# Kernel optimization log

Hardware: AMD Instinct MI355X
Metric: run time of the kernel (lower is better)

## Reference

```python
import jax, jax.numpy as jnp
import numpy as np

LN_EPS = 1e-5


def _layernorm(x, gamma, beta):
    mu = jnp.mean(x, axis=-1, keepdims=True)
    var = jnp.mean(jnp.square(x - mu), axis=-1, keepdims=True)
    return (x - mu) * jax.lax.rsqrt(var + LN_EPS) * gamma + beta


def setup_inputs() -> dict:
    key = jax.random.key(0)
    ks = jax.random.split(key, 8)
    B, T, C, H, HS = 8, 2048, 384, 6, 64
    s = C ** -0.5
    return {
        "x": jax.random.normal(ks[0], (B, T, C), jnp.float32),
        "wq": jax.random.normal(ks[1], (H, C, HS), jnp.float32) * s,
        "wk": jax.random.normal(ks[2], (H, C, HS), jnp.float32) * s,
        "wv": jax.random.normal(ks[3], (H, C, HS), jnp.float32) * s,
        "w_proj": jax.random.normal(ks[4], (C, C), jnp.float32) * s,
        "b_proj": jnp.zeros((C,), jnp.float32),
        "w1": jax.random.normal(ks[5], (C, 4 * C), jnp.float32) * s,
        "b1": jnp.zeros((4 * C,), jnp.float32),
        "w2": jax.random.normal(ks[6], (4 * C, C), jnp.float32) * (4 * C) ** -0.5,
        "b2": jnp.zeros((C,), jnp.float32),
        "g1": jnp.ones((C,), jnp.float32),
        "be1": jnp.zeros((C,), jnp.float32),
        "g2": jnp.ones((C,), jnp.float32),
        "be2": jnp.zeros((C,), jnp.float32),
    }


def reference(x, wq, wk, wv, w_proj, b_proj, w1, b1, w2, b2, g1, be1, g2, be2):
    B, T, C = x.shape
    HS = wq.shape[-1]
    # --- multi-head causal self-attention (per-head linear, concat, proj) ---
    q = jnp.einsum("btc,hcd->bhtd", x, wq)
    k = jnp.einsum("btc,hcd->bhtd", x, wk)
    v = jnp.einsum("btc,hcd->bhtd", x, wv)
    scores = jnp.einsum("bhtd,bhsd->bhts", q, k) * (HS ** -0.5)
    causal = jnp.tril(jnp.ones((T, T), bool))
    scores = jnp.where(causal, scores, -jnp.inf)
    att = jax.nn.softmax(scores, axis=-1)  # dropout = identity (eval)
    o = jnp.einsum("bhts,bhsd->bhtd", att, v)
    o = o.transpose(0, 2, 1, 3).reshape(B, T, C)  # concat heads
    sa = o @ w_proj + b_proj
    # --- post-LN residual ---
    x = _layernorm(x + sa, g1, be1)
    # --- feed-forward ---
    ff = jax.nn.relu(x @ w1 + b1) @ w2 + b2
    x = _layernorm(x + ff, g2, be2)
    return x
```

## Files before the change

### kernel.cpp

```cpp
#include <hip/hip_runtime.h>

typedef unsigned short u16;
typedef unsigned int u32;
typedef u16 u16x4 __attribute__((ext_vector_type(4)));
typedef u16 u16x8 __attribute__((ext_vector_type(8)));
typedef u32 u32x4 __attribute__((ext_vector_type(4)));
typedef __bf16 bf16v8 __attribute__((ext_vector_type(8)));
typedef float f32x4 __attribute__((ext_vector_type(4)));
typedef float f32x2 __attribute__((ext_vector_type(2)));

#define DEV __device__ __forceinline__

DEV u16 f2bf(float f) {
  union { float f; u32 u; } v; v.f = f;
  u32 r = v.u + 0x7fffu + ((v.u >> 16) & 1u);
  return (u16)(r >> 16);
}
DEV float bf2f(u16 u) { union { u32 u; float f; } v; v.u = ((u32)u) << 16; return v.f; }

DEV u32 cvtpk(float a, float b) {
  u32 d;
  asm("v_cvt_pk_bf16_f32 %0, %1, %2" : "=v"(d) : "v"(a), "v"(b));
  return d;
}

DEV f32x4 mfma16(u16x8 a, u16x8 b, f32x4 c) {
  return __builtin_amdgcn_mfma_f32_16x16x32_bf16(
      __builtin_bit_cast(bf16v8, a), __builtin_bit_cast(bf16v8, b), c, 0, 0, 0);
}

typedef const __attribute__((address_space(1))) void* gas_ptr;
typedef __attribute__((address_space(3))) void* las_ptr;
#define GLOAD16(GP, LP) __builtin_amdgcn_global_load_lds((gas_ptr)(GP), (las_ptr)(LP), 16, 0, 0)

__global__ __launch_bounds__(256) void cast_x_kernel(const float* __restrict__ x,
                                                     u16* __restrict__ xb) {
  int i = blockIdx.x * 256 + threadIdx.x;
  const f32x4* p = (const f32x4*)x;
  f32x4 a = p[2 * i], b = p[2 * i + 1];
  u16x8 o;
  #pragma unroll
  for (int j = 0; j < 4; ++j) { o[j] = f2bf(a[j]); o[4 + j] = f2bf(b[j]); }
  *((u16x8*)xb + i) = o;
}

__global__ __launch_bounds__(256) void prep_w_kernel(
    const float* __restrict__ wq, const float* __restrict__ wk,
    const float* __restrict__ wv, const float* __restrict__ wproj,
    const float* __restrict__ w1, const float* __restrict__ w2,
    u16* __restrict__ wqkvt, u16* __restrict__ wprojt,
    u16* __restrict__ w1t, u16* __restrict__ w2t) {
  int idx = blockIdx.x * 256 + threadIdx.x;
  if (idx < 442368) {
    int n = idx / 384, c = idx % 384;
    int which = n / 384;
    int hd = n % 384;
    int h = hd >> 6, d = hd & 63;
    const float* src = (which == 0) ? wq : ((which == 1) ? wk : wv);
    wqkvt[idx] = f2bf(src[((size_t)h * 384 + c) * 64 + d]);
  } else if (idx < 442368 + 147456) {
    int e = idx - 442368;
    int n = e / 384, c = e % 384;
    wprojt[e] = f2bf(wproj[(size_t)c * 384 + n]);
  } else if (idx < 442368 + 147456 + 589824) {
    int e = idx - (442368 + 147456);
    int n = e / 384, c = e % 384;
    w1t[e] = f2bf(w1[(size_t)c * 1536 + n]);
  } else {
    int e = idx - (442368 + 147456 + 589824);
    int n = e / 1536, c = e % 1536;
    w2t[e] = f2bf(w2[(size_t)c * 384 + n]);
  }
}

template <int K, int BM, int EPI>
__global__ __launch_bounds__(256) void gemm_kernel(
    const u16* __restrict__ A, const u16* __restrict__ Bt, const int N,
    const float* __restrict__ bias, const float* __restrict__ resf,
    const u16* __restrict__ resb, void* __restrict__ outv, void* __restrict__ outv2) {
  constexpr int NF = (BM == 128) ? 4 : 2;
  constexpr int AC = BM / 32;
  __shared__ u16 As[BM * 64];
  __shared__ u16 Bs[128 * 64];
  const int t = threadIdx.x;
  const int w = t >> 6, l = t & 63, l15 = l & 15, lg = l >> 4;
  const int wrow = (BM == 128) ? (w >> 1) * 64 : 0;
  const int wcol = (BM == 128) ? (w & 1) * 64 : w * 32;
  const int m0 = blockIdx.x * BM, n0 = blockIdx.y * 128;
  const int lr8 = l >> 3;
  const int su = (l & 7) ^ lr8;
  const u16* gA = A + (size_t)(m0 + lr8) * K + su * 8;
  const u16* gB = Bt + (size_t)(n0 + lr8) * K + su * 8;

  f32x4 acc[4][NF];
  #pragma unroll
  for (int i = 0; i < 4; ++i)
    #pragma unroll
    for (int j = 0; j < NF; ++j) acc[i][j] = (f32x4){0.f, 0.f, 0.f, 0.f};

  constexpr int NT = K / 64;
  #pragma unroll 1
  for (int kt = 0; kt < NT; ++kt) {
    #pragma unroll
    for (int c = 0; c < AC; ++c)
      GLOAD16(gA + (size_t)(w * (BM / 4) + c * 8) * K + kt * 64,
              (char*)As + w * (BM * 32) + c * 1024);
    #pragma unroll
    for (int c = 0; c < 4; ++c)
      GLOAD16(gB + (size_t)(w * 32 + c * 8) * K + kt * 64,
              (char*)Bs + w * 4096 + c * 1024);
    __syncthreads();
    u16x8 af[4][2], bfr[NF][2];
    #pragma unroll
    for (int i = 0; i < 4; ++i) {
      const int row = wrow + i * 16 + l15;
      #pragma unroll
      for (int ks = 0; ks < 2; ++ks)
        af[i][ks] = *(const u16x8*)&As[row * 64 + ((4 * ks + lg) ^ (row & 7)) * 8];
    }
    #pragma unroll
    for (int j = 0; j < NF; ++j) {
      const int row = wcol + j * 16 + l15;
      #pragma unroll
      for (int ks = 0; ks < 2; ++ks)
        bfr[j][ks] = *(const u16x8*)&Bs[row * 64 + ((4 * ks + lg) ^ (row & 7)) * 8];
    }
    #pragma unroll
    for (int ks = 0; ks < 2; ++ks)
      #pragma unroll
      for (int mi = 0; mi < 4; ++mi)
        #pragma unroll
        for (int ni = 0; ni < NF; ++ni)
          acc[mi][ni] = mfma16(af[mi][ks], bfr[ni][ks], acc[mi][ni]);
    __syncthreads();
  }

  #pragma unroll
  for (int mi = 0; mi < 4; ++mi) {
    #pragma unroll
    for (int ni = 0; ni < NF; ++ni) {
      const int rowg = m0 + wrow + mi * 16 + lg * 4;
      const int colg = n0 + wcol + ni * 16 + l15;
      if constexpr (EPI == 0) {
        if (n0 < 768) {
          #pragma unroll
          for (int r = 0; r < 4; ++r)
            ((u16*)outv)[(size_t)(rowg + r) * 768 + colg] = f2bf(acc[mi][ni][r]);
        } else {
          const int hd = colg - 768;
          u16x4 pv;
          #pragma unroll
          for (int r = 0; r < 4; ++r) pv[r] = f2bf(acc[mi][ni][r]);
          *(u16x4*)((u16*)outv2 + (size_t)((rowg >> 11) * 6 + (hd >> 6)) * 131072 +
                    (size_t)(hd & 63) * 2048 + (rowg & 2047)) = pv;
        }
      } else {
        const float b_ = bias[colg];
        #pragma unroll
        for (int r = 0; r < 4; ++r) {
          float v = acc[mi][ni][r];
          const size_t oi = (size_t)(rowg + r) * N + colg;
          if constexpr (EPI == 1) {
            ((float*)outv)[oi] = v + b_ + resf[oi];
          } else if constexpr (EPI == 2) {
            ((u16*)outv)[oi] = f2bf(fmaxf(v + b_, 0.f));
          } else {
            ((float*)outv)[oi] = v + b_ + bf2f(resb[oi]);
          }
        }
      }
    }
  }
}

__global__ __launch_bounds__(256, 5) void attn_kernel(const u16* __restrict__ qk,
                                                      const u16* __restrict__ vt,
                                                      u16* __restrict__ o,
                                                      float* __restrict__ part) {
  __shared__ __align__(16) char smem[32768];

  const int t = threadIdx.x;
  const int w = t >> 6, l = t & 63, l15 = l & 15, lg = l >> 4;
  const int idx = blockIdx.x;
  const int hl = idx % 48;
  const int g = idx / 48;
  int qt, k0, k1, e = 0;
  bool heavy;
  if (g < 32) {
    heavy = true; e = g;
    qt = 31 - (g >> 1);
    const int kmid = (qt + 1) >> 1;
    if (g & 1) { k0 = kmid; k1 = qt + 1; } else { k0 = 0; k1 = kmid; }
  } else {
    heavy = false; qt = 47 - g; k0 = 0; k1 = qt + 1;
  }
  const int b = hl / 6, head = hl % 6;
  const float SC = 0.125f * 1.44269504f;
  const float FM = 17.312340f;

  u16x8 qf[2];
  {
    const u16* qp = qk + (size_t)b * 2048 * 768 +
                    (size_t)(qt * 64 + w * 16 + l15) * 768 + head * 64 + lg * 8;
    qf[0] = *(const u16x8*)qp;
    qf[1] = *(const u16x8*)(qp + 32);
  }
  u16x8 ones;
  #pragma unroll
  for (int j = 0; j < 8; ++j) ones[j] = 0x3F80;

  f32x4 Oa[4];
  f32x4 Osum = (f32x4){0.f, 0.f, 0.f, 0.f};
  #pragma unroll
  for (int i = 0; i < 4; ++i) Oa[i] = (f32x4){0.f, 0.f, 0.f, 0.f};

  const int su16 = ((l & 7) ^ (l >> 3)) << 4;
  const char* kg0 = (const char*)qk + (size_t)b * 2048 * 1536 +
                    (size_t)(w * 8 + (l >> 3)) * 1536 + (size_t)(384 + head * 64) * 2 + su16;
  const char* vg0 = (const char*)vt + (size_t)(b * 6 + head) * 262144 +
                    (size_t)(w * 8 + (l >> 3)) * 4096 + su16;

  auto stage = [&](int kt, int bufsel) {
    const char* kg = kg0 + (size_t)kt * 98304;
    const char* vg = vg0 + (size_t)kt * 128;
    char* kl = smem + bufsel * 8192 + w * 1024;
    char* vl = smem + 16384 + bufsel * 8192 + w * 1024;
    GLOAD16(kg, kl);
    GLOAD16(kg + 49152, kl + 4096);
    GLOAD16(vg, vl);
    GLOAD16(vg + 131072, vl + 4096);
  };

  auto compute = [&](int bufoff, bool diag) {
    f32x4 sa[4];
    __builtin_amdgcn_s_setprio(1);
    #pragma unroll
    for (int st = 0; st < 4; ++st) {
      sa[st] = (f32x4){0.f, 0.f, 0.f, 0.f};
      const int sr = st * 16 + l15;
      #pragma unroll
      for (int ks = 0; ks < 2; ++ks) {
        u16x8 kf = *(const u16x8*)(smem + bufoff + sr * 128 +
                                   (((ks * 4 + lg) ^ (sr & 7)) << 4));
        sa[st] = mfma16(kf, qf[ks], sa[st]);
      }
    }
    __builtin_amdgcn_s_setprio(0);
    if (diag) {
      #pragma unroll
      for (int st = 0; st < 4; ++st)
        #pragma unroll
        for (int r = 0; r < 4; ++r)
          if (st * 16 + lg * 4 + r > w * 16 + l15) sa[st][r] = -3.0e38f;
    }
    u32 pk2[4][2];
    #pragma unroll
    for (int st = 0; st < 4; ++st) {
      float e0 = exp2f(sa[st][0] * SC - FM);
      float e1 = exp2f(sa[st][1] * SC - FM);
      float e2 = exp2f(sa[st][2] * SC - FM);
      float e3 = exp2f(sa[st][3] * SC - FM);
      pk2[st][0] = cvtpk(e0, e1);
      pk2[st][1] = cvtpk(e2, e3);
    }
    #pragma unroll
    for (int ks = 0; ks < 2; ++ks) {
      u32 wds[4];
      #pragma unroll
      for (int wd = 0; wd < 4; ++wd) {
        int src = ((2 * (lg & 1) + (wd >> 1)) << 4) | l15;
        u32 c0 = (u32)__shfl((int)pk2[2 * ks][wd & 1], src);
        u32 c1 = (u32)__shfl((int)pk2[2 * ks + 1][wd & 1], src);
        wds[wd] = (lg & 2) ? c1 : c0;
      }
      u16x8 pf = __builtin_bit_cast(u16x8, (u32x4){wds[0], wds[1], wds[2], wds[3]});
      __builtin_amdgcn_s_setprio(1);
      #pragma unroll
      for (int dt = 0; dt < 4; ++dt) {
        const int dd = dt * 16 + l15;
        u16x8 vf = *(const u16x8*)(smem + 16384 + bufoff + dd * 128 +
                                   (((ks * 4 + lg) ^ (dd & 7)) << 4));
        Oa[dt] = mfma16(pf, vf, Oa[dt]);
      }
      Osum = mfma16(pf, ones, Osum);
      __builtin_amdgcn_s_setprio(0);
    }
  };

  int cur = 0;
  stage(k0, 0);
  #pragma unroll 1
  for (int kt = k0; kt < k1; ++kt) {
    __syncthreads();
    if (kt + 1 < k1) stage(kt + 1, cur ^ 1);
    compute(cur * 8192, kt == qt);
    cur ^= 1;
  }

  if (!heavy) {
    float inv[4];
    #pragma unroll
    for (int r = 0; r < 4; ++r) inv[r] = 1.0f / Osum[r];
    #pragma unroll
    for (int dt = 0; dt < 4; ++dt)
      #pragma unroll
      for (int r = 0; r < 4; ++r) {
        size_t row = (size_t)b * 2048 + qt * 64 + w * 16 + lg * 4 + r;
        o[row * 384 + head * 64 + dt * 16 + l15] = f2bf(Oa[dt][r] * inv[r]);
      }
  } else {
    float* slot = part + (size_t)(hl * 32 + e) * 4224;
    if (l15 == 0) {
      #pragma unroll
      for (int r = 0; r < 4; ++r) slot[w * 16 + lg * 4 + r] = Osum[r];
    }
    #pragma unroll
    for (int dt = 0; dt < 4; ++dt)
      #pragma unroll
      for (int r = 0; r < 4; ++r)
        slot[128 + (w * 16 + lg * 4 + r) * 64 + dt * 16 + l15] = Oa[dt][r];
  }
}

__global__ __launch_bounds__(256) void attn_combine_kernel(const float* __restrict__ part,
                                                           u16* __restrict__ o) {
  const int idx = blockIdx.x;
  const int hl = idx % 48;
  const int qt = 31 - idx / 48;
  const int e0 = (31 - qt) * 2;
  const float* s0 = part + (size_t)(hl * 32 + e0) * 4224;
  const float* s1 = s0 + 4224;
  const int t = threadIdx.x;
  const int row = t >> 2, c0 = (t & 3) * 16;
  const float inv = 1.0f / (s0[row] + s1[row]);
  const int b = hl / 6, head = hl % 6;
  const f32x4* a0 = (const f32x4*)(s0 + 128 + row * 64 + c0);
  const f32x4* a1 = (const f32x4*)(s1 + 128 + row * 64 + c0);
  u32 wv[8];
  #pragma unroll
  for (int j = 0; j < 4; ++j) {
    f32x4 va = a0[j], vb = a1[j];
    float y0 = (va[0] + vb[0]) * inv;
    float y1 = (va[1] + vb[1]) * inv;
    float y2 = (va[2] + vb[2]) * inv;
    float y3 = (va[3] + vb[3]) * inv;
    wv[2 * j] = cvtpk(y0, y1);
    wv[2 * j + 1] = cvtpk(y2, y3);
  }
  u16* op = o + ((size_t)(b * 2048 + qt * 64 + row)) * 384 + head * 64 + c0;
  *(u32x4*)op = (u32x4){wv[0], wv[1], wv[2], wv[3]};
  *(u32x4*)(op + 8) = (u32x4){wv[4], wv[5], wv[6], wv[7]};
}

template <int OUT_BF16>
__global__ __launch_bounds__(256) void ln_kernel(const float* __restrict__ in,
                                                 const float* __restrict__ g,
                                                 const float* __restrict__ be,
                                                 void* __restrict__ outv) {
  const int row = blockIdx.x * 4 + (threadIdx.x >> 6);
  const int lane = threadIdx.x & 63;
  const float* p = in + (size_t)row * 384 + lane * 6;
  float v[6];
  {
    const f32x2* p2 = (const f32x2*)p;
    f32x2 a0 = p2[0], a1 = p2[1], a2 = p2[2];
    v[0] = a0[0]; v[1] = a0[1]; v[2] = a1[0]; v[3] = a1[1]; v[4] = a2[0]; v[5] = a2[1];
  }
  float s = v[0] + v[1] + v[2] + v[3] + v[4] + v[5];
  #pragma unroll
  for (int m = 1; m < 64; m <<= 1) s += __shfl_xor(s, m, 64);
  const float mu = s * (1.0f / 384.0f);
  float d2 = 0.f;
  #pragma unroll
  for (int j = 0; j < 6; ++j) { float d = v[j] - mu; d2 += d * d; }
  #pragma unroll
  for (int m = 1; m < 64; m <<= 1) d2 += __shfl_xor(d2, m, 64);
  const float rstd = rsqrtf(d2 * (1.0f / 384.0f) + 1e-5f);
  const int c = lane * 6;
  float y[6];
  #pragma unroll
  for (int j = 0; j < 6; ++j) y[j] = (v[j] - mu) * rstd * g[c + j] + be[c + j];
  if constexpr (OUT_BF16) {
    u32* ob = (u32*)((u16*)outv + (size_t)row * 384 + c);
    #pragma unroll
    for (int j = 0; j < 3; ++j)
      ob[j] = (u32)f2bf(y[2 * j]) | ((u32)f2bf(y[2 * j + 1]) << 16);
  } else {
    float* of = (float*)outv + (size_t)row * 384 + c;
    f32x2* o2 = (f32x2*)of;
    #pragma unroll
    for (int j = 0; j < 3; ++j) o2[j] = (f32x2){y[2 * j], y[2 * j + 1]};
  }
}

extern "C" void kernel_launch(void* const* d_in, const int* in_sizes, int n_in,
                              void* d_out, int out_size, void* d_ws, size_t ws_size,
                              hipStream_t stream) {
  const float* x     = (const float*)d_in[0];
  const float* wq    = (const float*)d_in[1];
  const float* wk    = (const float*)d_in[2];
  const float* wv    = (const float*)d_in[3];
  const float* wproj = (const float*)d_in[4];
  const float* bproj = (const float*)d_in[5];
  const float* w1    = (const float*)d_in[6];
  const float* b1    = (const float*)d_in[7];
  const float* w2    = (const float*)d_in[8];
  const float* b2    = (const float*)d_in[9];
  const float* g1    = (const float*)d_in[10];
  const float* be1   = (const float*)d_in[11];
  const float* g2    = (const float*)d_in[12];
  const float* be2   = (const float*)d_in[13];

  char* ws = (char*)d_ws;
  u16*   xb    = (u16*)(ws + 0);
  u16*   qk    = (u16*)(ws + 12582912);
  u16*   vt    = (u16*)(ws + 37748736);
  u16*   obuf  = (u16*)(ws + 50331648);
  float* res1  = (float*)(ws + 62914560);
  u16*   x1b   = (u16*)(ws + 88080384);
  u16*   wqkvt = (u16*)(ws + 100663296);
  u16*   wprjt = (u16*)(ws + 101548032);
  u16*   w1t   = (u16*)(ws + 101842944);
  u16*   w2t   = (u16*)(ws + 103022592);
  u16*   h1    = qk;
  float* part  = res1;

  cast_x_kernel<<<3072, 256, 0, stream>>>(x, xb);
  prep_w_kernel<<<6912, 256, 0, stream>>>(wq, wk, wv, wproj, w1, w2, wqkvt, wprjt, w1t, w2t);
  gemm_kernel<384, 128, 0><<<dim3(128, 9), 256, 0, stream>>>(xb, wqkvt, 768, nullptr, nullptr, nullptr, qk, vt);
  attn_kernel<<<2304, 256, 0, stream>>>(qk, vt, obuf, part);
  attn_combine_kernel<<<768, 256, 0, stream>>>(part, obuf);
  gemm_kernel<384, 64, 1><<<dim3(256, 3), 256, 0, stream>>>(obuf, wprjt, 384, bproj, x, nullptr, res1, nullptr);
  ln_kernel<1><<<4096, 256, 0, stream>>>(res1, g1, be1, x1b);
  gemm_kernel<384, 128, 2><<<dim3(128, 12), 256, 0, stream>>>(x1b, w1t, 1536, b1, nullptr, nullptr, h1, nullptr);
  gemm_kernel<1536, 64, 3><<<dim3(256, 3), 256, 0, stream>>>(h1, w2t, 384, b2, nullptr, x1b, res1, nullptr);
  ln_kernel<0><<<4096, 256, 0, stream>>>(res1, g2, be2, d_out);
}
```

Measured before the change: 209.2 us.

## Double-buffer GEMM LDS tiles and use 64-row tiles for all GEMMs

```diff
diff --git a/kernel.cpp b/kernel.cpp
--- a/kernel.cpp
+++ b/kernel.cpp
@@ -73,73 +73,78 @@
   }
 }
 
-template <int K, int BM, int EPI>
+template <int K, int EPI>
 __global__ __launch_bounds__(256) void gemm_kernel(
     const u16* __restrict__ A, const u16* __restrict__ Bt, const int N,
     const float* __restrict__ bias, const float* __restrict__ resf,
     const u16* __restrict__ resb, void* __restrict__ outv, void* __restrict__ outv2) {
-  constexpr int NF = (BM == 128) ? 4 : 2;
-  constexpr int AC = BM / 32;
-  __shared__ u16 As[BM * 64];
-  __shared__ u16 Bs[128 * 64];
+  __shared__ u16 As[2 * 64 * 64];
+  __shared__ u16 Bs[2 * 128 * 64];
   const int t = threadIdx.x;
   const int w = t >> 6, l = t & 63, l15 = l & 15, lg = l >> 4;
-  const int wrow = (BM == 128) ? (w >> 1) * 64 : 0;
-  const int wcol = (BM == 128) ? (w & 1) * 64 : w * 32;
-  const int m0 = blockIdx.x * BM, n0 = blockIdx.y * 128;
+  const int wcol = w * 32;
+  const int m0 = blockIdx.x * 64, n0 = blockIdx.y * 128;
   const int lr8 = l >> 3;
   const int su = (l & 7) ^ lr8;
   const u16* gA = A + (size_t)(m0 + lr8) * K + su * 8;
   const u16* gB = Bt + (size_t)(n0 + lr8) * K + su * 8;
 
-  f32x4 acc[4][NF];
+  f32x4 acc[4][2];
   #pragma unroll
   for (int i = 0; i < 4; ++i)
     #pragma unroll
-    for (int j = 0; j < NF; ++j) acc[i][j] = (f32x4){0.f, 0.f, 0.f, 0.f};
+    for (int j = 0; j < 2; ++j) acc[i][j] = (f32x4){0.f, 0.f, 0.f, 0.f};
+
+  auto stage = [&](int kt, int buf) {
+    #pragma unroll
+    for (int c = 0; c < 2; ++c)
+      GLOAD16(gA + (size_t)(w * 16 + c * 8) * K + kt * 64,
+              (char*)As + buf * 8192 + w * 2048 + c * 1024);
+    #pragma unroll
+    for (int c = 0; c < 4; ++c)
+      GLOAD16(gB + (size_t)(w * 32 + c * 8) * K + kt * 64,
+              (char*)Bs + buf * 16384 + w * 4096 + c * 1024);
+  };
 
   constexpr int NT = K / 64;
+  int cur = 0;
+  stage(0, 0);
   #pragma unroll 1
   for (int kt = 0; kt < NT; ++kt) {
-    #pragma unroll
-    for (int c = 0; c < AC; ++c)
-      GLOAD16(gA + (size_t)(w * (BM / 4) + c * 8) * K + kt * 64,
-              (char*)As + w * (BM * 32) + c * 1024);
-    #pragma unroll
-    for (int c = 0; c < 4; ++c)
-      GLOAD16(gB + (size_t)(w * 32 + c * 8) * K + kt * 64,
-              (char*)Bs + w * 4096 + c * 1024);
     __syncthreads();
-    u16x8 af[4][2], bfr[NF][2];
+    if (kt + 1 < NT) stage(kt + 1, cur ^ 1);
+    const u16* Ab = As + cur * 4096;
+    const u16* Bb = Bs + cur * 8192;
+    u16x8 af[4][2], bfr[2][2];
     #pragma unroll
     for (int i = 0; i < 4; ++i) {
-      const int row = wrow + i * 16 + l15;
+      const int row = i * 16 + l15;
       #pragma unroll
       for (int ks = 0; ks < 2; ++ks)
-        af[i][ks] = *(const u16x8*)&As[row * 64 + ((4 * ks + lg) ^ (row & 7)) * 8];
-    }
-    #pragma unroll
-    for (int j = 0; j < NF; ++j) {
+        af[i][ks] = *(const u16x8*)&Ab[row * 64 + (((4 * ks + lg) ^ (row & 7)) << 3)];
+    }
+    #pragma unroll
+    for (int j = 0; j < 2; ++j) {
       const int row = wcol + j * 16 + l15;
       #pragma unroll
       for (int ks = 0; ks < 2; ++ks)
-        bfr[j][ks] = *(const u16x8*)&Bs[row * 64 + ((4 * ks + lg) ^ (row & 7)) * 8];
+        bfr[j][ks] = *(const u16x8*)&Bb[row * 64 + (((4 * ks + lg) ^ (row & 7)) << 3)];
     }
     #pragma unroll
     for (int ks = 0; ks < 2; ++ks)
       #pragma unroll
       for (int mi = 0; mi < 4; ++mi)
         #pragma unroll
-        for (int ni = 0; ni < NF; ++ni)
+        for (int ni = 0; ni < 2; ++ni)
           acc[mi][ni] = mfma16(af[mi][ks], bfr[ni][ks], acc[mi][ni]);
-    __syncthreads();
+    cur ^= 1;
   }
 
   #pragma unroll
   for (int mi = 0; mi < 4; ++mi) {
     #pragma unroll
-    for (int ni = 0; ni < NF; ++ni) {
-      const int rowg = m0 + wrow + mi * 16 + lg * 4;
+    for (int ni = 0; ni < 2; ++ni) {
+      const int rowg = m0 + mi * 16 + lg * 4;
       const int colg = n0 + wcol + ni * 16 + l15;
       if constexpr (EPI == 0) {
         if (n0 < 768) {
@@ -427,12 +432,12 @@
 
   cast_x_kernel<<<3072, 256, 0, stream>>>(x, xb);
   prep_w_kernel<<<6912, 256, 0, stream>>>(wq, wk, wv, wproj, w1, w2, wqkvt, wprjt, w1t, w2t);
-  gemm_kernel<384, 128, 0><<<dim3(128, 9), 256, 0, stream>>>(xb, wqkvt, 768, nullptr, nullptr, nullptr, qk, vt);
+  gemm_kernel<384, 0><<<dim3(256, 9), 256, 0, stream>>>(xb, wqkvt, 768, nullptr, nullptr, nullptr, qk, vt);
   attn_kernel<<<2304, 256, 0, stream>>>(qk, vt, obuf, part);
   attn_combine_kernel<<<768, 256, 0, stream>>>(part, obuf);
-  gemm_kernel<384, 64, 1><<<dim3(256, 3), 256, 0, stream>>>(obuf, wprjt, 384, bproj, x, nullptr, res1, nullptr);
+  gemm_kernel<384, 1><<<dim3(256, 3), 256, 0, stream>>>(obuf, wprjt, 384, bproj, x, nullptr, res1, nullptr);
   ln_kernel<1><<<4096, 256, 0, stream>>>(res1, g1, be1, x1b);
-  gemm_kernel<384, 128, 2><<<dim3(128, 12), 256, 0, stream>>>(x1b, w1t, 1536, b1, nullptr, nullptr, h1, nullptr);
-  gemm_kernel<1536, 64, 3><<<dim3(256, 3), 256, 0, stream>>>(h1, w2t, 384, b2, nullptr, x1b, res1, nullptr);
+  gemm_kernel<384, 2><<<dim3(256, 12), 256, 0, stream>>>(x1b, w1t, 1536, b1, nullptr, nullptr, h1, nullptr);
+  gemm_kernel<1536, 3><<<dim3(256, 3), 256, 0, stream>>>(h1, w2t, 384, b2, nullptr, x1b, res1, nullptr);
   ln_kernel<0><<<4096, 256, 0, stream>>>(res1, g2, be2, d_out);
 }
```

After: 207.7 us. No clear change (-0.7%).
